# Optimization experiments

Hardware: AMD Instinct MI355X
Metric: run time of the kernel (lower is better)

The kernel has to match this reference:

```python
import jax, jax.numpy as jnp
import numpy as np

N = 20000
E = 640000
H, C = 4, 64
L = 3
B = 16
EPS = 1e-5


def setup_inputs() -> dict:
    key = jax.random.key(0)
    ks = jax.random.split(key, 12)
    x = jax.random.normal(ks[0], (N, 256), dtype=jnp.float32)
    edge_index = jax.random.randint(ks[1], (2, E), 0, N, dtype=jnp.int64)
    batch = jnp.sort(jax.random.randint(ks[2], (N,), 0, B, dtype=jnp.int64))
    s = 0.05
    return {
        "x": x,
        "edge_index": edge_index,
        "batch": batch,
        "Wl": jax.random.normal(ks[3], (L, 256, H * C), dtype=jnp.float32) * s,
        "bl": jnp.zeros((L, H * C), dtype=jnp.float32),
        "Wr": jax.random.normal(ks[4], (L, 256, H * C), dtype=jnp.float32) * s,
        "br": jnp.zeros((L, H * C), dtype=jnp.float32),
        "att": jax.random.normal(ks[5], (L, H, C), dtype=jnp.float32) * s,
        "conv_bias": jnp.zeros((L, H * C), dtype=jnp.float32),
        "prelu_a": jnp.full((L,), 0.25, dtype=jnp.float32),
        "norm_w": jnp.ones((H * C,), dtype=jnp.float32),
        "norm_b": jnp.zeros((H * C,), dtype=jnp.float32),
        "norm_alpha": jnp.ones((H * C,), dtype=jnp.float32),
        "fc_W": jax.random.normal(ks[6], (H * C, 128), dtype=jnp.float32) * s,
        "fc_b": jnp.zeros((128,), dtype=jnp.float32),
    }


def graph_norm(h, w, b, alpha):
    # GraphNorm with batch=None: all rows form one segment (as in source forward)
    mean = jnp.mean(h, axis=0, keepdims=True)
    shifted = h - alpha * mean
    var = jnp.mean(shifted * shifted, axis=0, keepdims=True)
    return w * shifted / jnp.sqrt(var + EPS) + b


def gatv2_layer(h, src, dst, Wl, bl, Wr, br, att, bias):
    xl = (h @ Wl + bl).reshape(N, H, C)  # source transform
    xr = (h @ Wr + br).reshape(N, H, C)  # target transform
    m = jax.nn.leaky_relu(xl[src] + xr[dst], negative_slope=0.2)  # [Etot,H,C]
    e = jnp.einsum("ehc,hc->eh", m, att)  # [Etot,H]
    emax = jax.ops.segment_max(e, dst, num_segments=N)  # self-loops guarantee coverage
    ex = jnp.exp(e - emax[dst])
    denom = jax.ops.segment_sum(ex, dst, num_segments=N)
    alpha = ex / denom[dst]
    out = jax.ops.segment_sum(alpha[:, :, None] * xl[src], dst, num_segments=N)
    return out.reshape(N, H * C) + bias


def reference(x, edge_index, batch, Wl, bl, Wr, br, att, conv_bias, prelu_a,
              norm_w, norm_b, norm_alpha, fc_W, fc_b):
    loop = jnp.arange(N, dtype=edge_index.dtype)
    src = jnp.concatenate([edge_index[0], loop])  # add self-loops (PyG default)
    dst = jnp.concatenate([edge_index[1], loop])
    h = x
    for l in range(L):
        h = gatv2_layer(h, src, dst, Wl[l], bl[l], Wr[l], br[l], att[l], conv_bias[l])
        h = graph_norm(h, norm_w, norm_b, norm_alpha)
        h = jnp.where(h >= 0, h, prelu_a[l] * h)  # PReLU; dropout is identity in eval
    pooled = jax.ops.segment_sum(h, batch, num_segments=B)  # global_add_pool
    pooled = graph_norm(pooled, norm_w, norm_b, norm_alpha)  # shared norm reused after pool
    return pooled @ fc_W + fc_b
```

## Files before the change

kernel.cpp:

```cpp
#include <hip/hip_runtime.h>
#include <math.h>

#define N_NODES 20000
#define N_EDGES 640000
#define ETOT (N_EDGES + N_NODES)
#define HC 256
#define NLAYER 3
#define NBATCH 16
#define GEPS 1e-5f
#define NSLOT 64
#define L2E 1.44269504f

typedef unsigned short u16;
typedef unsigned int u32;
typedef __attribute__((ext_vector_type(8))) short short8;
typedef __attribute__((ext_vector_type(4))) float floatx4;

__device__ __forceinline__ u16 f2bf(float f) {
    u32 u = __float_as_uint(f);
    u32 r = (u + 0x7FFFu + ((u >> 16) & 1u)) >> 16;
    return (u16)r;
}

__device__ __forceinline__ float4 bf2f4(uint2 u) {
    float4 r;
    r.x = __uint_as_float(u.x << 16);
    r.y = __uint_as_float(u.x & 0xFFFF0000u);
    r.z = __uint_as_float(u.y << 16);
    r.w = __uint_as_float(u.y & 0xFFFF0000u);
    return r;
}

__device__ __forceinline__ float dpp_red16(float x) {
    x += __int_as_float(__builtin_amdgcn_update_dpp(0, __float_as_int(x), 0xB1, 0xF, 0xF, true));
    x += __int_as_float(__builtin_amdgcn_update_dpp(0, __float_as_int(x), 0x4E, 0xF, 0xF, true));
    x += __int_as_float(__builtin_amdgcn_update_dpp(0, __float_as_int(x), 0x141, 0xF, 0xF, true));
    x += __int_as_float(__builtin_amdgcn_update_dpp(0, __float_as_int(x), 0x140, 0xF, 0xF, true));
    return x;
}



__global__ __launch_bounds__(256) void prep(const float* __restrict__ x, u16* __restrict__ xbf,
                                            const float* __restrict__ Wl, const float* __restrict__ Wr,
                                            u16* __restrict__ WT, uint4* __restrict__ zbase, int zq) {
    __shared__ float T[32][33];
    int b = blockIdx.x, tid = threadIdx.x;
    if (b < 1250) {
        int rt = b;
        int wid = tid >> 6, lane = tid & 63;
        int row = rt * 16 + (lane & 15);
        int q8 = (lane >> 4) * 8;
        #pragma unroll
        for (int kk = 0; kk < 2; ++kk) {
            int kt = wid + kk * 4;
            int kcol = kt * 32 + q8;
            const float4* px = (const float4*)(x + (size_t)row * 256 + kcol);
            float4 a = px[0], c = px[1];
            u16 o[8] = {f2bf(a.x), f2bf(a.y), f2bf(a.z), f2bf(a.w),
                        f2bf(c.x), f2bf(c.y), f2bf(c.z), f2bf(c.w)};
            *(uint4*)(xbf + (((size_t)rt * 8 + kt) * 64 + lane) * 8) = *(const uint4*)o;
        }
    } else if (b < 1634) {
        int bi = b - 1250;
        int kb = bi & 7;
        int nb = (bi >> 3) & 15;
        int l = bi >> 7;
        int n0 = nb * 32, k0 = kb * 32;
        const float* W = ((n0 < 256) ? Wl : Wr) + (size_t)l * 65536;
        int nn0 = n0 & 255;
        int tx = tid & 31, ty = tid >> 5;
        #pragma unroll
        for (int i = 0; i < 4; ++i)
            T[ty + i * 8][tx] = W[(size_t)(k0 + ty + i * 8) * 256 + nn0 + tx];
        __syncthreads();
        int lane = tid & 63, jp = (tid >> 6) & 1, cl = tid >> 7;
        int ct = n0 / 16 + cl;
        u16 o4[4];
        #pragma unroll
        for (int jj = 0; jj < 4; ++jj)
            o4[jj] = f2bf(T[(lane >> 4) * 8 + jp * 4 + jj][cl * 16 + (lane & 15)]);
        u16* outw = WT + (size_t)l * 131072;
        *(uint2*)(outw + (((size_t)ct * 8 + kb) * 64 + lane) * 8 + jp * 4) = *(const uint2*)o4;
    } else {
        uint4 z = make_uint4(0, 0, 0, 0);
        for (int i = (b - 1634) * 256 + tid; i < zq; i += 120 * 256) zbase[i] = z;
    }
}


__global__ void count_deg(const int* __restrict__ dst, int* __restrict__ deg) {
    int e = blockIdx.x * 256 + threadIdx.x;
    if (e < N_EDGES) atomicAdd(&deg[dst[e]], 1);
}

__global__ __launch_bounds__(1024) void scan_excl(int* __restrict__ data, int* __restrict__ cursor) {
    __shared__ int wsum[16];
    int t = threadIdx.x, lane = t & 63, wid = t >> 6;
    int i0 = t * 20;
    int d[20];
    int tot = 0;
    #pragma unroll
    for (int j = 0; j < 20; ++j) {
        int i = i0 + j;
        int v = (i < N_NODES) ? (data[i] + 1) : 0;
        d[j] = v;
        tot += v;
    }
    int x = tot;
    #pragma unroll
    for (int off = 1; off < 64; off <<= 1) {
        int tmp = __shfl_up(x, off);
        if (lane >= off) x += tmp;
    }
    if (lane == 63) wsum[wid] = x;
    __syncthreads();
    if (t == 0) {
        int run = 0;
        #pragma unroll
        for (int w = 0; w < 16; ++w) { int tv = wsum[w]; wsum[w] = run; run += tv; }
    }
    __syncthreads();
    int run = wsum[wid] + x - tot;
    #pragma unroll
    for (int j = 0; j < 20; ++j) {
        int i = i0 + j;
        if (i < N_NODES) { data[i] = run; cursor[i] = run; }
        run += d[j];
    }
    if (t == 0) data[N_NODES] = ETOT;
}

__global__ void scatter_edges(const int* __restrict__ src, const int* __restrict__ dst,
                              int* __restrict__ cursor, int* __restrict__ col) {
    int t = blockIdx.x * 256 + threadIdx.x;
    if (t < N_NODES) {
        int p = atomicAdd(&cursor[t], 1);
        col[p] = t;
    } else if (t < N_NODES + N_EDGES) {
        int e = t - N_NODES;
        int p = atomicAdd(&cursor[dst[e]], 1);
        col[p] = src[e];
    }
}


__global__ __launch_bounds__(256) void gemm_mfma(
    const u16* __restrict__ At, const u16* __restrict__ WTt,
    const float* __restrict__ b0, const float* __restrict__ b1,
    u16* __restrict__ xlb, u16* __restrict__ xrb) {
    int row0 = blockIdx.x * 128;
    int strip = blockIdx.y;
    const float* bias = (strip < 2) ? b0 : b1;
    u16* outp = (strip < 2) ? xlb : xrb;
    int c0 = (strip & 1) * 128;

    int tid = threadIdx.x;
    int wave = tid >> 6, lane = tid & 63;
    int wm = (wave & 1) * 64, wn = (wave >> 1) * 64;
    int quad = lane >> 4, l16 = lane & 15;
    int rt0 = (row0 + wm) >> 4;
    int ct0 = (strip * 128 + wn) >> 4;

    floatx4 acc[4][4] = {};
    const u16* pA[4];
    const u16* pB[4];
    #pragma unroll
    for (int mi = 0; mi < 4; ++mi) {
        int rt = min(rt0 + mi, 1249);
        pA[mi] = At + ((size_t)rt * 8) * 512 + lane * 8;
    }
    #pragma unroll
    for (int ni = 0; ni < 4; ++ni)
        pB[ni] = WTt + ((size_t)(ct0 + ni) * 8) * 512 + lane * 8;

    #pragma unroll
    for (int kt = 0; kt < 8; ++kt) {
        short8 af[4], bf[4];
        #pragma unroll
        for (int mi = 0; mi < 4; ++mi) af[mi] = *(const short8*)(pA[mi] + kt * 512);
        #pragma unroll
        for (int ni = 0; ni < 4; ++ni) bf[ni] = *(const short8*)(pB[ni] + kt * 512);
        #pragma unroll
        for (int mi = 0; mi < 4; ++mi)
            #pragma unroll
            for (int ni = 0; ni < 4; ++ni)
                acc[mi][ni] = __builtin_amdgcn_mfma_f32_16x16x32_bf16(af[mi], bf[ni], acc[mi][ni], 0, 0, 0);
    }

    #pragma unroll
    for (int ni = 0; ni < 4; ++ni) {
        int col = c0 + wn + ni * 16 + l16;
        float bv = bias[col];
        #pragma unroll
        for (int mi = 0; mi < 4; ++mi) {
            int gr = row0 + wm + mi * 16 + quad * 4;
            #pragma unroll
            for (int r = 0; r < 4; ++r) {
                if (gr + r < N_NODES)
                    outp[(size_t)(gr + r) * 256 + col] = f2bf(acc[mi][ni][r] + bv);
            }
        }
    }
}


__global__ __launch_bounds__(512) void gat_agg(
    const u16* __restrict__ xlb, const u16* __restrict__ xrb,
    const int* __restrict__ rowptr, const int* __restrict__ col,
    const float* __restrict__ att_l, const float* __restrict__ bias_l,
    u16* __restrict__ hB, float* __restrict__ slot) {
    __shared__ float pden[8][64];
    __shared__ float4 pacc[8][64];
    __shared__ float sred[4][520];
    int wid = threadIdx.x >> 6, lane = threadIdx.x & 63;
    int nw = wid >> 1, half = wid & 1;
    int node = blockIdx.x * 4 + nw;
    const uint2* xl2 = (const uint2*)xlb;
    float4 attv = ((const float4*)att_l)[lane];
    attv.x *= L2E; attv.y *= L2E; attv.z *= L2E; attv.w *= L2E;
    float4 xrv = bf2f4(((const uint2*)xrb)[(size_t)node * 64 + lane]);
    int beg = rowptr[node], end = rowptr[node + 1];
    int mid = (beg + end) >> 1;
    int j0 = half ? mid : beg;
    int j1 = half ? end : mid;

    float denom = 0.f;
    float4 acc = make_float4(0.f, 0.f, 0.f, 0.f);

    int j = j0;
    for (; j + 8 <= j1; j += 8) {
        int s[8];
        uint2 raw[8];
        float4 a[8];
        float p[8];
        #pragma unroll
        for (int u = 0; u < 8; ++u) s[u] = col[j + u];
        #pragma unroll
        for (int u = 0; u < 8; ++u) raw[u] = xl2[(size_t)s[u] * 64 + lane];
        #pragma unroll
        for (int u = 0; u < 8; ++u) {
            a[u] = bf2f4(raw[u]);
            float vx = a[u].x + xrv.x, vy = a[u].y + xrv.y;
            float vz = a[u].z + xrv.z, vw = a[u].w + xrv.w;
            vx = fmaxf(vx, 0.2f * vx);
            vy = fmaxf(vy, 0.2f * vy);
            vz = fmaxf(vz, 0.2f * vz);
            vw = fmaxf(vw, 0.2f * vw);
            p[u] = vx * attv.x + vy * attv.y + vz * attv.z + vw * attv.w;
        }
        #pragma unroll
        for (int u = 0; u < 8; ++u) p[u] = dpp_red16(p[u]);
        #pragma unroll
        for (int u = 0; u < 8; ++u) {
            float w = exp2f(p[u]);
            denom += w;
            acc.x += w * a[u].x; acc.y += w * a[u].y;
            acc.z += w * a[u].z; acc.w += w * a[u].w;
        }
    }
    for (; j < j1; ++j) {
        int s = col[j];
        float4 a = bf2f4(xl2[(size_t)s * 64 + lane]);
        float vx = a.x + xrv.x, vy = a.y + xrv.y;
        float vz = a.z + xrv.z, vw = a.w + xrv.w;
        vx = fmaxf(vx, 0.2f * vx);
        vy = fmaxf(vy, 0.2f * vy);
        vz = fmaxf(vz, 0.2f * vz);
        vw = fmaxf(vw, 0.2f * vw);
        float p = vx * attv.x + vy * attv.y + vz * attv.z + vw * attv.w;
        p = dpp_red16(p);
        float w = exp2f(p);
        denom += w;
        acc.x += w * a.x; acc.y += w * a.y; acc.z += w * a.z; acc.w += w * a.w;
    }

    if (half == 1) {
        pden[wid][lane] = denom;
        pacc[wid][lane] = acc;
    }
    __syncthreads();
    if (half == 0) {
        denom += pden[wid + 1][lane];
        float4 o2 = pacc[wid + 1][lane];
        acc.x += o2.x; acc.y += o2.y; acc.z += o2.z; acc.w += o2.w;
        float inv = 1.f / denom;
        float4 b4 = ((const float4*)bias_l)[lane];
        float4 o;
        o.x = acc.x * inv + b4.x; o.y = acc.y * inv + b4.y;
        o.z = acc.z * inv + b4.z; o.w = acc.w * inv + b4.w;
        u16 ob[4] = {f2bf(o.x), f2bf(o.y), f2bf(o.z), f2bf(o.w)};
        ((uint2*)hB)[(size_t)node * 64 + lane] = *(const uint2*)ob;
        int cb2 = lane * 4;
        sred[nw][cb2 + 0] = o.x; sred[nw][cb2 + 1] = o.y;
        sred[nw][cb2 + 2] = o.z; sred[nw][cb2 + 3] = o.w;
        sred[nw][256 + cb2 + 0] = o.x * o.x; sred[nw][256 + cb2 + 1] = o.y * o.y;
        sred[nw][256 + cb2 + 2] = o.z * o.z; sred[nw][256 + cb2 + 3] = o.w * o.w;
    }
    __syncthreads();
    int t = threadIdx.x;
    float s = sred[0][t] + sred[1][t] + sred[2][t] + sred[3][t];
    atomicAdd(&slot[(blockIdx.x & (NSLOT - 1)) * 512 + t], s);
}


__global__ __launch_bounds__(256) void fin_stats(const float* __restrict__ slot,
                                                 const float* __restrict__ nw, const float* __restrict__ nb,
                                                 const float* __restrict__ na,
                                                 float* __restrict__ wcbb) {
    int c = threadIdx.x;
    float sum = 0.f, sq = 0.f;
    for (int s = 0; s < NSLOT; ++s) {
        sum += slot[s * 512 + c];
        sq += slot[s * 512 + 256 + c];
    }
    const float invn = 1.f / (float)N_NODES;
    float mean = sum * invn, Eh2 = sq * invn;
    float a = na[c];
    float var = Eh2 - (2.f * a - a * a) * mean * mean;
    float wc = nw[c] * rsqrtf(var + GEPS);
    wcbb[c] = wc;
    wcbb[256 + c] = nb[c] - a * mean * wc;
}


__global__ __launch_bounds__(256) void norm_prelu(const u16* __restrict__ hB, u16* __restrict__ hbfT,
                                                  const float* __restrict__ wcbb,
                                                  const float* __restrict__ pa, int l) {
    int rt = blockIdx.x;
    int wid = threadIdx.x >> 6, lane = threadIdx.x & 63;
    float ap = pa[l];
    int row = rt * 16 + (lane & 15);
    int q8 = (lane >> 4) * 8;
    #pragma unroll
    for (int kk = 0; kk < 2; ++kk) {
        int kt = wid + kk * 4;
        int kcol = kt * 32 + q8;
        uint4 raw = *(const uint4*)(hB + (size_t)row * 256 + kcol);
        float4 a = bf2f4(make_uint2(raw.x, raw.y));
        float4 b = bf2f4(make_uint2(raw.z, raw.w));
        float4 wc0 = *(const float4*)&wcbb[kcol];
        float4 wc1 = *(const float4*)&wcbb[kcol + 4];
        float4 bb0 = *(const float4*)&wcbb[256 + kcol];
        float4 bb1 = *(const float4*)&wcbb[256 + kcol + 4];
        a.x = a.x * wc0.x + bb0.x; a.y = a.y * wc0.y + bb0.y;
        a.z = a.z * wc0.z + bb0.z; a.w = a.w * wc0.w + bb0.w;
        b.x = b.x * wc1.x + bb1.x; b.y = b.y * wc1.y + bb1.y;
        b.z = b.z * wc1.z + bb1.z; b.w = b.w * wc1.w + bb1.w;
        a.x = fmaxf(a.x, ap * a.x); a.y = fmaxf(a.y, ap * a.y);
        a.z = fmaxf(a.z, ap * a.z); a.w = fmaxf(a.w, ap * a.w);
        b.x = fmaxf(b.x, ap * b.x); b.y = fmaxf(b.y, ap * b.y);
        b.z = fmaxf(b.z, ap * b.z); b.w = fmaxf(b.w, ap * b.w);
        u16 o[8] = {f2bf(a.x), f2bf(a.y), f2bf(a.z), f2bf(a.w),
                    f2bf(b.x), f2bf(b.y), f2bf(b.z), f2bf(b.w)};
        *(uint4*)(hbfT + (((size_t)rt * 8 + kt) * 64 + lane) * 8) = *(const uint4*)o;
    }
}


__global__ __launch_bounds__(256) void pool_kernel(const u16* __restrict__ hB,
                                                   const int* __restrict__ batch,
                                                   const float* __restrict__ slots2,
                                                   const float* __restrict__ nw, const float* __restrict__ nb,
                                                   const float* __restrict__ na, const float* __restrict__ pa,
                                                   float* __restrict__ pooled) {
    __shared__ float accs[NBATCH][256];
    int c = threadIdx.x;
    float sum = 0.f, sq = 0.f;
    for (int s = 0; s < NSLOT; ++s) {
        sum += slots2[s * 512 + c];
        sq += slots2[s * 512 + 256 + c];
    }
    const float invn = 1.f / (float)N_NODES;
    float mean = sum * invn, Eh2 = sq * invn;
    float a = na[c];
    float var = Eh2 - (2.f * a - a * a) * mean * mean;
    float wc = nw[c] * rsqrtf(var + GEPS);
    float bb = nb[c] - a * mean * wc;
    float ap = pa[2];

    #pragma unroll
    for (int b = 0; b < NBATCH; ++b) accs[b][c] = 0.f;
    int r0 = blockIdx.x * 100;
    int r1 = min(N_NODES, r0 + 100);
    for (int i = r0; i < r1; ++i) {
        float v = __uint_as_float(((u32)hB[(size_t)i * 256 + c]) << 16);
        v = v * wc + bb;
        v = fmaxf(v, ap * v);
        accs[batch[i]][c] += v;
    }
    int bmin = batch[r0], bmax = batch[r1 - 1];
    for (int b = bmin; b <= bmax; ++b) atomicAdd(&pooled[b * 256 + c], accs[b][c]);
}


__global__ __launch_bounds__(256) void poolnorm_fc(const float* __restrict__ pooled,
                                                   const float* __restrict__ nw, const float* __restrict__ nb,
                                                   const float* __restrict__ na,
                                                   const float* __restrict__ fcW, const float* __restrict__ fcb,
                                                   float* __restrict__ out) {
    __shared__ float pn[256];
    __shared__ float part[128];
    int b = blockIdx.x;
    int c = threadIdx.x;
    float mean = 0.f, sq = 0.f;
    #pragma unroll
    for (int i = 0; i < NBATCH; ++i) {
        float v = pooled[i * 256 + c];
        mean += v; sq += v * v;
    }
    mean *= (1.f / NBATCH); sq *= (1.f / NBATCH);
    float a = na[c];
    float var = sq - (2.f * a - a * a) * mean * mean;
    float wc = nw[c] * rsqrtf(var + GEPS);
    float bb = nb[c] - a * mean * wc;
    pn[c] = pooled[b * 256 + c] * wc + bb;
    __syncthreads();
    int o = c & 127, half = c >> 7;
    float s = 0.f;
    int kbase = half * 128;
    #pragma unroll 8
    for (int k = 0; k < 128; ++k)
        s += pn[kbase + k] * fcW[(kbase + k) * 128 + o];
    if (half == 1) part[o] = s;
    __syncthreads();
    if (half == 0) out[b * 128 + o] = s + part[o] + fcb[o];
}


extern "C" void kernel_launch(void* const* d_in, const int* in_sizes, int n_in,
                              void* d_out, int out_size, void* d_ws, size_t ws_size,
                              hipStream_t stream) {
    const float* x    = (const float*)d_in[0];
    const int*   ei   = (const int*)d_in[1];
    const int*   batch= (const int*)d_in[2];
    const float* Wl   = (const float*)d_in[3];
    const float* bl   = (const float*)d_in[4];
    const float* Wr   = (const float*)d_in[5];
    const float* br   = (const float*)d_in[6];
    const float* att  = (const float*)d_in[7];
    const float* cb   = (const float*)d_in[8];
    const float* pa   = (const float*)d_in[9];
    const float* nw   = (const float*)d_in[10];
    const float* nb   = (const float*)d_in[11];
    const float* na   = (const float*)d_in[12];
    const float* fcW  = (const float*)d_in[13];
    const float* fcb  = (const float*)d_in[14];
    float* out = (float*)d_out;

    char* ws = (char*)d_ws;
    size_t off = 0;
    auto carve = [&](size_t bytes) -> void* {
        void* p = (void*)(ws + off);
        off += (bytes + 255) & ~(size_t)255;
        return p;
    };
    size_t z0 = off;
    int*   rowptr = (int*)carve((N_NODES + 1) * sizeof(int));
    float* slots  = (float*)carve((size_t)NLAYER * NSLOT * 512 * sizeof(float));
    float* pooled = (float*)carve(NBATCH * HC * sizeof(float));
    size_t z1 = off;
    int*   cursor = (int*)carve(N_NODES * sizeof(int));
    int*   colidx = (int*)carve((size_t)ETOT * sizeof(int));
    u16*   xlb    = (u16*)carve((size_t)N_NODES * HC * sizeof(u16));
    u16*   xrb    = (u16*)carve((size_t)N_NODES * HC * sizeof(u16));
    u16*   hB     = (u16*)carve((size_t)N_NODES * HC * sizeof(u16));
    u16*   xbf    = (u16*)carve((size_t)N_NODES * HC * sizeof(u16));
    u16*   hbf    = (u16*)carve((size_t)N_NODES * HC * sizeof(u16));
    u16*   WT     = (u16*)carve((size_t)NLAYER * 512 * 256 * sizeof(u16));
    float* wcbb   = (float*)carve(512 * sizeof(float));

    int zq = (int)((z1 - z0) / 16);
    const int* srcp = ei;
    const int* dstp = ei + N_EDGES;

    prep<<<1754, 256, 0, stream>>>(x, xbf, Wl, Wr, WT, (uint4*)(ws + z0), zq);
    count_deg<<<(N_EDGES + 255) / 256, 256, 0, stream>>>(dstp, rowptr);
    scan_excl<<<1, 1024, 0, stream>>>(rowptr, cursor);
    scatter_edges<<<(ETOT + 255) / 256, 256, 0, stream>>>(srcp, dstp, cursor, colidx);

    for (int l = 0; l < NLAYER; ++l) {
        const u16* Asrc = (l == 0) ? xbf : hbf;
        gemm_mfma<<<dim3(157, 4), 256, 0, stream>>>(Asrc, WT + (size_t)l * 131072,
                                                    bl + l * 256, br + l * 256, xlb, xrb);
        gat_agg<<<5000, 512, 0, stream>>>(xlb, xrb, rowptr, colidx, att + l * 256, cb + l * 256,
                                          hB, slots + (size_t)l * NSLOT * 512);
        if (l < NLAYER - 1) {
            fin_stats<<<1, 256, 0, stream>>>(slots + (size_t)l * NSLOT * 512, nw, nb, na, wcbb);
            norm_prelu<<<1250, 256, 0, stream>>>(hB, hbf, wcbb, pa, l);
        }
    }
    pool_kernel<<<200, 256, 0, stream>>>(hB, batch, slots + (size_t)2 * NSLOT * 512,
                                         nw, nb, na, pa, pooled);
    poolnorm_fc<<<16, 256, 0, stream>>>(pooled, nw, nb, na, fcW, fcb, out);
}
```

Baseline: 548.1 us.

## Retile GEMM to full-width row blocks with LDS-staged stores; one wave per node in aggregation

The GEMM now gives each block 64 rows across all 512 output columns (xl and xr together), with each wave owning 128 columns. Results are staged through shared memory so that global stores become coalesced 16-byte row writes instead of scattered 2-byte stores. The aggregation kernel drops the two-wave split per node and uses one wave per node with 256-thread blocks, removing the LDS partial merge and its extra sync. The trade-offs are higher register pressure in the GEMM (launch bounds with one block), fewer GEMM blocks, and less parallelism per high-degree node in aggregation.

Result: faster. 504.1 us (-8.0%).

```diff
diff --git a/kernel.cpp b/kernel.cpp
--- a/kernel.cpp
+++ b/kernel.cpp
@@ -145,91 +145,100 @@
 }
 
 
-__global__ __launch_bounds__(256) void gemm_mfma(
+__global__ __launch_bounds__(256, 1) void gemm_mfma(
     const u16* __restrict__ At, const u16* __restrict__ WTt,
     const float* __restrict__ b0, const float* __restrict__ b1,
     u16* __restrict__ xlb, u16* __restrict__ xrb) {
-    int row0 = blockIdx.x * 128;
-    int strip = blockIdx.y;
-    const float* bias = (strip < 2) ? b0 : b1;
-    u16* outp = (strip < 2) ? xlb : xrb;
-    int c0 = (strip & 1) * 128;
-
+    __shared__ u16 tile[32][520];
+    int row0 = blockIdx.x * 64;
     int tid = threadIdx.x;
     int wave = tid >> 6, lane = tid & 63;
-    int wm = (wave & 1) * 64, wn = (wave >> 1) * 64;
     int quad = lane >> 4, l16 = lane & 15;
-    int rt0 = (row0 + wm) >> 4;
-    int ct0 = (strip * 128 + wn) >> 4;
-
-    floatx4 acc[4][4] = {};
+    int rt0 = row0 >> 4;
+    int ct0 = wave * 8;
+
+    floatx4 acc[4][8] = {};
     const u16* pA[4];
-    const u16* pB[4];
+    const u16* pB[8];
     #pragma unroll
     for (int mi = 0; mi < 4; ++mi) {
         int rt = min(rt0 + mi, 1249);
-        pA[mi] = At + ((size_t)rt * 8) * 512 + lane * 8;
-    }
-    #pragma unroll
-    for (int ni = 0; ni < 4; ++ni)
-        pB[ni] = WTt + ((size_t)(ct0 + ni) * 8) * 512 + lane * 8;
+        pA[mi] = At + (size_t)rt * 4096 + lane * 8;
+    }
+    #pragma unroll
+    for (int ni = 0; ni < 8; ++ni)
+        pB[ni] = WTt + (size_t)(ct0 + ni) * 4096 + lane * 8;
 
     #pragma unroll
     for (int kt = 0; kt < 8; ++kt) {
-        short8 af[4], bf[4];
+        short8 af[4], bf[8];
         #pragma unroll
         for (int mi = 0; mi < 4; ++mi) af[mi] = *(const short8*)(pA[mi] + kt * 512);
         #pragma unroll
-        for (int ni = 0; ni < 4; ++ni) bf[ni] = *(const short8*)(pB[ni] + kt * 512);
+        for (int ni = 0; ni < 8; ++ni) bf[ni] = *(const short8*)(pB[ni] + kt * 512);
         #pragma unroll
         for (int mi = 0; mi < 4; ++mi)
             #pragma unroll
-            for (int ni = 0; ni < 4; ++ni)
+            for (int ni = 0; ni < 8; ++ni)
                 acc[mi][ni] = __builtin_amdgcn_mfma_f32_16x16x32_bf16(af[mi], bf[ni], acc[mi][ni], 0, 0, 0);
     }
 
-    #pragma unroll
-    for (int ni = 0; ni < 4; ++ni) {
-        int col = c0 + wn + ni * 16 + l16;
-        float bv = bias[col];
-        #pragma unroll
-        for (int mi = 0; mi < 4; ++mi) {
-            int gr = row0 + wm + mi * 16 + quad * 4;
+    float bv[8];
+    #pragma unroll
+    for (int ni = 0; ni < 8; ++ni) {
+        int c = wave * 128 + ni * 16 + l16;
+        bv[ni] = (c < 256) ? b0[c] : b1[c - 256];
+    }
+
+    #pragma unroll
+    for (int pass = 0; pass < 2; ++pass) {
+        #pragma unroll
+        for (int mi = 0; mi < 2; ++mi) {
+            int lrow = mi * 16 + quad * 4;
             #pragma unroll
-            for (int r = 0; r < 4; ++r) {
-                if (gr + r < N_NODES)
-                    outp[(size_t)(gr + r) * 256 + col] = f2bf(acc[mi][ni][r] + bv);
+            for (int ni = 0; ni < 8; ++ni) {
+                int c = wave * 128 + ni * 16 + l16;
+                #pragma unroll
+                for (int r = 0; r < 4; ++r)
+                    tile[lrow + r][c] = f2bf(acc[pass * 2 + mi][ni][r] + bv[ni]);
             }
         }
-    }
-}
-
-
-__global__ __launch_bounds__(512) void gat_agg(
+        __syncthreads();
+        #pragma unroll
+        for (int iter = 0; iter < 8; ++iter) {
+            int lrow = iter * 4 + wave;
+            int gr = row0 + pass * 32 + lrow;
+            if (gr < N_NODES) {
+                if (lane < 32)
+                    *(uint4*)(xlb + (size_t)gr * 256 + lane * 8) = *(const uint4*)&tile[lrow][lane * 8];
+                else
+                    *(uint4*)(xrb + (size_t)gr * 256 + (lane - 32) * 8) = *(const uint4*)&tile[lrow][256 + (lane - 32) * 8];
+            }
+        }
+        __syncthreads();
+    }
+}
+
+
+__global__ __launch_bounds__(256) void gat_agg(
     const u16* __restrict__ xlb, const u16* __restrict__ xrb,
     const int* __restrict__ rowptr, const int* __restrict__ col,
     const float* __restrict__ att_l, const float* __restrict__ bias_l,
     u16* __restrict__ hB, float* __restrict__ slot) {
-    __shared__ float pden[8][64];
-    __shared__ float4 pacc[8][64];
     __shared__ float sred[4][520];
     int wid = threadIdx.x >> 6, lane = threadIdx.x & 63;
-    int nw = wid >> 1, half = wid & 1;
-    int node = blockIdx.x * 4 + nw;
+    int node = blockIdx.x * 4 + wid;
     const uint2* xl2 = (const uint2*)xlb;
     float4 attv = ((const float4*)att_l)[lane];
     attv.x *= L2E; attv.y *= L2E; attv.z *= L2E; attv.w *= L2E;
     float4 xrv = bf2f4(((const uint2*)xrb)[(size_t)node * 64 + lane]);
     int beg = rowptr[node], end = rowptr[node + 1];
-    int mid = (beg + end) >> 1;
-    int j0 = half ? mid : beg;
-    int j1 = half ? end : mid;
 
     float denom = 0.f;
     float4 acc = make_float4(0.f, 0.f, 0.f, 0.f);
 
-    int j = j0;
-    for (; j + 8 <= j1; j += 8) {
+    int j = beg;
+    for (; j + 8 <= end; j += 8) {
         int s[8];
         uint2 raw[8];
         float4 a[8];
@@ -259,7 +268,7 @@
             acc.z += w * a[u].z; acc.w += w * a[u].w;
         }
     }
-    for (; j < j1; ++j) {
+    for (; j < end; ++j) {
         int s = col[j];
         float4 a = bf2f4(xl2[(size_t)s * 64 + lane]);
         float vx = a.x + xrv.x, vy = a.y + xrv.y;
@@ -275,32 +284,27 @@
         acc.x += w * a.x; acc.y += w * a.y; acc.z += w * a.z; acc.w += w * a.w;
     }
 
-    if (half == 1) {
-        pden[wid][lane] = denom;
-        pacc[wid][lane] = acc;
-    }
-    __syncthreads();
-    if (half == 0) {
-        denom += pden[wid + 1][lane];
-        float4 o2 = pacc[wid + 1][lane];
-        acc.x += o2.x; acc.y += o2.y; acc.z += o2.z; acc.w += o2.w;
-        float inv = 1.f / denom;
-        float4 b4 = ((const float4*)bias_l)[lane];
-        float4 o;
-        o.x = acc.x * inv + b4.x; o.y = acc.y * inv + b4.y;
-        o.z = acc.z * inv + b4.z; o.w = acc.w * inv + b4.w;
-        u16 ob[4] = {f2bf(o.x), f2bf(o.y), f2bf(o.z), f2bf(o.w)};
-        ((uint2*)hB)[(size_t)node * 64 + lane] = *(const uint2*)ob;
-        int cb2 = lane * 4;
-        sred[nw][cb2 + 0] = o.x; sred[nw][cb2 + 1] = o.y;
-        sred[nw][cb2 + 2] = o.z; sred[nw][cb2 + 3] = o.w;
-        sred[nw][256 + cb2 + 0] = o.x * o.x; sred[nw][256 + cb2 + 1] = o.y * o.y;
-        sred[nw][256 + cb2 + 2] = o.z * o.z; sred[nw][256 + cb2 + 3] = o.w * o.w;
-    }
+    float inv = 1.f / denom;
+    float4 b4 = ((const float4*)bias_l)[lane];
+    float4 o;
+    o.x = acc.x * inv + b4.x; o.y = acc.y * inv + b4.y;
+    o.z = acc.z * inv + b4.z; o.w = acc.w * inv + b4.w;
+    u16 ob[4] = {f2bf(o.x), f2bf(o.y), f2bf(o.z), f2bf(o.w)};
+    ((uint2*)hB)[(size_t)node * 64 + lane] = *(const uint2*)ob;
+
+    int cb2 = lane * 4;
+    sred[wid][cb2 + 0] = o.x; sred[wid][cb2 + 1] = o.y;
+    sred[wid][cb2 + 2] = o.z; sred[wid][cb2 + 3] = o.w;
+    sred[wid][256 + cb2 + 0] = o.x * o.x; sred[wid][256 + cb2 + 1] = o.y * o.y;
+    sred[wid][256 + cb2 + 2] = o.z * o.z; sred[wid][256 + cb2 + 3] = o.w * o.w;
     __syncthreads();
     int t = threadIdx.x;
-    float s = sred[0][t] + sred[1][t] + sred[2][t] + sred[3][t];
-    atomicAdd(&slot[(blockIdx.x & (NSLOT - 1)) * 512 + t], s);
+    #pragma unroll
+    for (int h = 0; h < 2; ++h) {
+        int idx = t + h * 256;
+        float s = sred[0][idx] + sred[1][idx] + sred[2][idx] + sred[3][idx];
+        atomicAdd(&slot[(blockIdx.x & (NSLOT - 1)) * 512 + idx], s);
+    }
 }
 
 
@@ -481,9 +485,9 @@
 
     for (int l = 0; l < NLAYER; ++l) {
         const u16* Asrc = (l == 0) ? xbf : hbf;
-        gemm_mfma<<<dim3(157, 4), 256, 0, stream>>>(Asrc, WT + (size_t)l * 131072,
-                                                    bl + l * 256, br + l * 256, xlb, xrb);
-        gat_agg<<<5000, 512, 0, stream>>>(xlb, xrb, rowptr, colidx, att + l * 256, cb + l * 256,
+        gemm_mfma<<<313, 256, 0, stream>>>(Asrc, WT + (size_t)l * 131072,
+                                           bl + l * 256, br + l * 256, xlb, xrb);
+        gat_agg<<<5000, 256, 0, stream>>>(xlb, xrb, rowptr, colidx, att + l * 256, cb + l * 256,
                                           hB, slots + (size_t)l * NSLOT * 512);
         if (l < NLAYER - 1) {
             fin_stats<<<1, 256, 0, stream>>>(slots + (size_t)l * NSLOT * 512, nw, nb, na, wcbb);
```
